# Kernel tuning notes

Measured on AMD Instinct MI355X. Metric: run time of the kernel, lower is better.

## Reference

```python
import jax, jax.numpy as jnp
import numpy as np

# Production-scale dims (see shape_source)
N = 100000      # nodes
E = 1600000     # shortest-path edges
I = 128         # in_channels
O = 128         # out_channels
K = 5           # max_distance
BN_EPS = 1e-5
GIN_EPS = 0.0   # eps=0.0, trainable_eps=False


def setup_inputs() -> dict:
    key = jax.random.key(0)
    ks = jax.random.split(key, 10)
    node_embeddings = jax.random.normal(ks[0], (N, I), dtype=jnp.float32)
    edge_index = jax.random.randint(ks[1], (2, E), 0, N)          # [2, E] row/col
    edge_weights = jax.random.randint(ks[2], (E,), 1, K + 1)      # SP distance in 1..K
    hop_coef = jax.random.normal(ks[3], (K,), dtype=jnp.float32)
    W1 = jax.random.normal(ks[4], (I, O), dtype=jnp.float32) / np.sqrt(I).astype(np.float32)
    b1 = jnp.zeros((O,), jnp.float32)
    gamma1 = jnp.ones((O,), jnp.float32)
    beta1 = jnp.zeros((O,), jnp.float32)
    W2 = jax.random.normal(ks[5], (O, O), dtype=jnp.float32) / np.sqrt(O).astype(np.float32)
    b2 = jnp.zeros((O,), jnp.float32)
    gamma2 = jnp.ones((O,), jnp.float32)
    beta2 = jnp.zeros((O,), jnp.float32)
    return {
        "node_embeddings": node_embeddings,
        "edge_index": edge_index,
        "edge_weights": edge_weights,
        "hop_coef": hop_coef,
        "W1": W1, "b1": b1, "gamma1": gamma1, "beta1": beta1,
        "W2": W2, "b2": b2, "gamma2": gamma2, "beta2": beta2,
    }


def _batch_norm(x, gamma, beta):
    # BatchNorm1d in training mode: batch mean, biased batch variance
    mean = x.mean(axis=0)
    var = x.var(axis=0)
    return gamma * (x - mean) * jax.lax.rsqrt(var + BN_EPS) + beta


def reference(node_embeddings, edge_index, edge_weights, hop_coef,
              W1, b1, gamma1, beta1, W2, b2, gamma2, beta2):
    # Fused form of the per-hop loop: each edge with SP distance d contributes
    # softmax(hop_coef)[d-1] * x[col] to out[row]. Identical math to K separate
    # sparse.mm's weighted by hop_weights and summed.
    hop_w = jax.nn.softmax(hop_coef)                               # [K]
    valid = (edge_weights >= 1) & (edge_weights <= K)
    w_e = jnp.where(valid, hop_w[jnp.clip(edge_weights - 1, 0, K - 1)], 0.0)  # [E]
    row, col = edge_index[0], edge_index[1]
    msgs = w_e[:, None] * node_embeddings[col]                     # [E, I] gather
    agg = jnp.zeros_like(node_embeddings).at[row].add(msgs)        # [N, I] scatter-add
    h = (1.0 + GIN_EPS) * node_embeddings + agg                    # GIN combine
    h = jax.nn.relu(_batch_norm(h @ W1 + b1, gamma1, beta1))
    h = jax.nn.relu(_batch_norm(h @ W2 + b2, gamma2, beta2))
    return h
```

## Files before the change

### kernel.cpp

```cpp
#include <hip/hip_runtime.h>
#include <hip/hip_bf16.h>


#define RCAP 64
#define P2B 256
#define BPB 4

typedef __attribute__((ext_vector_type(8))) short short8;
typedef __attribute__((ext_vector_type(4))) float f32x4;

__device__ inline unsigned short f2bf(float v) {
    unsigned int u = __float_as_uint(v);
    return (unsigned short)((u + 0x7fffu + ((u >> 16) & 1u)) >> 16);
}
__device__ inline float bf2f(unsigned int u) { return __uint_as_float(u << 16); }
__device__ inline float bflo(unsigned int u) { return __uint_as_float(u << 16); }
__device__ inline float bfhi(unsigned int u) { return __uint_as_float(u & 0xFFFF0000u); }

__global__ __launch_bounds__(256) void prep_k(
        const float* __restrict__ hc, float* __restrict__ hwp, float* __restrict__ sums,
        const float* __restrict__ W1, const float* __restrict__ W2,
        unsigned short* __restrict__ w1h, unsigned short* __restrict__ w1l,
        unsigned short* __restrict__ w2h, unsigned short* __restrict__ w2l,
        const float4* __restrict__ x4, uint4* __restrict__ xb, int K, long long n8) {
    int b = blockIdx.x, tid = threadIdx.x;
    if (b == 0) {
        sums[tid] = 0.f; sums[tid + 256] = 0.f;
        if (tid == 0) {
            float tmp[8];
            float m = -1e30f;
            for (int k = 0; k < K; ++k) m = fmaxf(m, hc[k]);
            float s = 0.f;
            for (int k = 0; k < K; ++k) { float e = __expf(hc[k] - m); tmp[k] = e; s += e; }
            float inv = 1.f / s;
            for (int k = 0; k < 8; ++k) hwp[k] = 0.f;
            for (int k = 0; k < K; ++k) hwp[k + 1] = tmp[k] * inv;
        }
        return;
    }
    if (b <= 2) {
        const float* W = (b == 2) ? W2 : W1;
        unsigned short* th = (b == 2) ? w2h : w1h;
        unsigned short* tl = (b == 2) ? w2l : w1l;
        for (int i = tid; i < 16384; i += 256) {
            int k = i >> 7, n = i & 127;
            float v = W[k * 128 + n];
            unsigned short hi = f2bf(v);
            th[n * 128 + k] = hi;
            tl[n * 128 + k] = f2bf(v - bf2f(hi));
        }
        return;
    }
    long long g = (long long)(b - 3) * 256 + tid;
    if (g >= n8) return;
    float4 a = x4[g * 2], c = x4[g * 2 + 1];
    union { unsigned short us[8]; uint4 v; } o;
    o.us[0] = f2bf(a.x); o.us[1] = f2bf(a.y); o.us[2] = f2bf(a.z); o.us[3] = f2bf(a.w);
    o.us[4] = f2bf(c.x); o.us[5] = f2bf(c.y); o.us[6] = f2bf(c.z); o.us[7] = f2bf(c.w);
    xb[g] = o.v;
}

__global__ __launch_bounds__(256) void count_k(const int* __restrict__ rows,
        int* __restrict__ C, int E, int per, int nbukp) {
    __shared__ int hist[128];
    int blk = blockIdx.x, tid = threadIdx.x;
    for (int i = tid; i < nbukp; i += 256) hist[i] = 0;
    __syncthreads();
    int e0 = blk * per, e1 = min(E, e0 + per);
    for (int e = e0 + tid; e < e1; e += 256)
        atomicAdd(&hist[rows[e] >> 10], 1);
    __syncthreads();
    for (int i = tid; i < nbukp; i += 256) C[blk * nbukp + i] = hist[i];
}

__global__ __launch_bounds__(256) void scan1_k(int* __restrict__ C,
        int* __restrict__ tot, int nbukp, int nblk) {
    __shared__ int buf[256];
    int b = blockIdx.x, tid = threadIdx.x;
    int v = (tid < nblk) ? C[tid * nbukp + b] : 0;
    buf[tid] = v;
    __syncthreads();
#pragma unroll
    for (int off = 1; off < 256; off <<= 1) {
        int t = (tid >= off) ? buf[tid - off] : 0;
        __syncthreads();
        buf[tid] += t;
        __syncthreads();
    }
    if (tid < nblk) C[tid * nbukp + b] = buf[tid] - v;
    if (tid == 255) tot[b] = buf[255];
}

__global__ __launch_bounds__(256) void scan2_k(const int* __restrict__ tot,
        int* __restrict__ bstart, int nbukp) {
    __shared__ int s[129];
    int tid = threadIdx.x;
    if (tid < nbukp) s[tid] = tot[tid];
    __syncthreads();
    if (tid == 0) {
        int run = 0;
        for (int b = 0; b < nbukp; b++) { int t = s[b]; bstart[b] = run; run += t; }
        bstart[nbukp] = run;
    }
}

__global__ __launch_bounds__(256) void scatter_k(const int* __restrict__ rows,
        const int* __restrict__ cols, const int* __restrict__ ew,
        const int* __restrict__ O, const int* __restrict__ bstart,
        unsigned* __restrict__ bucketed, int E, int per, int nbukp, int K) {
    __shared__ unsigned curs[128];
    int blk = blockIdx.x, tid = threadIdx.x;
    for (int i = tid; i < nbukp; i += 256)
        curs[i] = (unsigned)(O[blk * nbukp + i] + bstart[i]);
    __syncthreads();
    int e0 = blk * per, e1 = min(E, e0 + per);
    for (int e = e0 + tid; e < e1; e += 256) {
        int r = rows[e];
        int c = cols[e];
        int d = ew[e];
        if (d < 1 || d > K) d = 0;
        unsigned idx = atomicAdd(&curs[r >> 10], 1u);
        bucketed[idx] = (unsigned)d | ((unsigned)c << 3) | ((unsigned)(r & 1023) << 20);
    }
}

__global__ __launch_bounds__(256) void slot3_k(const unsigned* __restrict__ bucketed,
        const int* __restrict__ bstart, const float* __restrict__ hwp,
        int* __restrict__ cur, int2* __restrict__ staging, int nbukp) {
    int bucket = blockIdx.x % nbukp, sub = blockIdx.x / nbukp;
    int s0 = bstart[bucket], s1 = bstart[bucket + 1];
    int cnt = s1 - s0;
    int qlo = s0 + (int)((long long)cnt * sub / BPB);
    int qhi = s0 + (int)((long long)cnt * (sub + 1) / BPB);
    int rbase = bucket << 10;
    for (int e = qlo + threadIdx.x; e < qhi; e += 256) {
        unsigned u = bucketed[e];
        int d = u & 7;
        int col = (u >> 3) & 0x1FFFF;
        int row = rbase + (int)(u >> 20);
        float w = hwp[d];
        int s = atomicAdd(&cur[row], 1);
        if (s < RCAP)
            staging[((size_t)row << 6) + s] = make_int2(col, __float_as_int(w));
    }
}

__global__ __launch_bounds__(256) void slot_k(const int* __restrict__ rows,
        const int* __restrict__ cols, const int* __restrict__ ew,
        const float* __restrict__ hwp, int* __restrict__ cur,
        int2* __restrict__ staging, int E, int K) {
    int e = blockIdx.x * 256 + threadIdx.x;
    if (e >= E) return;
    int r = rows[e];
    int d = ew[e];
    if (d < 1 || d > K) d = 0;
    float w = hwp[d];
    int s = atomicAdd(&cur[r], 1);
    if (s < RCAP)
        staging[((size_t)r << 6) + s] = make_int2(cols[e], __float_as_int(w));
}

__global__ __launch_bounds__(256) void gather_k(
        const unsigned short* __restrict__ xb, const int2* __restrict__ staging,
        const int* __restrict__ cur, unsigned short* __restrict__ h, int N) {
    int wid = (blockIdx.x * 256 + threadIdx.x) >> 6;
    if (wid >= N) return;
    int lane = threadIdx.x & 63;
    int g4 = lane >> 4, li = lane & 15;
    int deg = __builtin_amdgcn_readfirstlane(cur[wid]);
    deg = min(deg, RCAP);
    const int2* ep = staging + ((size_t)wid << 6);
    const unsigned short* xrow = xb + li * 8;
    float a0 = 0.f, a1 = 0.f, a2 = 0.f, a3 = 0.f;
    float a4 = 0.f, a5 = 0.f, a6 = 0.f, a7 = 0.f;
    if (g4 == 0) {
        uint4 u = *(const uint4*)(xb + (size_t)wid * 128 + li * 8);
        a0 = bflo(u.x); a1 = bfhi(u.x); a2 = bflo(u.y); a3 = bfhi(u.y);
        a4 = bflo(u.z); a5 = bfhi(u.z); a6 = bflo(u.w); a7 = bfhi(u.w);
    }
    int j = 0;
    for (; j + 16 <= deg; j += 16) {
        int2 p0 = ep[j + g4];
        int2 p1 = ep[j + 4 + g4];
        int2 p2 = ep[j + 8 + g4];
        int2 p3 = ep[j + 12 + g4];
        uint4 u0 = *(const uint4*)(xrow + (size_t)p0.x * 128);
        uint4 u1 = *(const uint4*)(xrow + (size_t)p1.x * 128);
        uint4 u2 = *(const uint4*)(xrow + (size_t)p2.x * 128);
        uint4 u3 = *(const uint4*)(xrow + (size_t)p3.x * 128);
        float w0 = __int_as_float(p0.y), w1 = __int_as_float(p1.y);
        float w2 = __int_as_float(p2.y), w3 = __int_as_float(p3.y);
        a0 = fmaf(w0, bflo(u0.x), a0); a1 = fmaf(w0, bfhi(u0.x), a1);
        a2 = fmaf(w0, bflo(u0.y), a2); a3 = fmaf(w0, bfhi(u0.y), a3);
        a4 = fmaf(w0, bflo(u0.z), a4); a5 = fmaf(w0, bfhi(u0.z), a5);
        a6 = fmaf(w0, bflo(u0.w), a6); a7 = fmaf(w0, bfhi(u0.w), a7);
        a0 = fmaf(w1, bflo(u1.x), a0); a1 = fmaf(w1, bfhi(u1.x), a1);
        a2 = fmaf(w1, bflo(u1.y), a2); a3 = fmaf(w1, bfhi(u1.y), a3);
        a4 = fmaf(w1, bflo(u1.z), a4); a5 = fmaf(w1, bfhi(u1.z), a5);
        a6 = fmaf(w1, bflo(u1.w), a6); a7 = fmaf(w1, bfhi(u1.w), a7);
        a0 = fmaf(w2, bflo(u2.x), a0); a1 = fmaf(w2, bfhi(u2.x), a1);
        a2 = fmaf(w2, bflo(u2.y), a2); a3 = fmaf(w2, bfhi(u2.y), a3);
        a4 = fmaf(w2, bflo(u2.z), a4); a5 = fmaf(w2, bfhi(u2.z), a5);
        a6 = fmaf(w2, bflo(u2.w), a6); a7 = fmaf(w2, bfhi(u2.w), a7);
        a0 = fmaf(w3, bflo(u3.x), a0); a1 = fmaf(w3, bfhi(u3.x), a1);
        a2 = fmaf(w3, bflo(u3.y), a2); a3 = fmaf(w3, bfhi(u3.y), a3);
        a4 = fmaf(w3, bflo(u3.z), a4); a5 = fmaf(w3, bfhi(u3.z), a5);
        a6 = fmaf(w3, bflo(u3.w), a6); a7 = fmaf(w3, bfhi(u3.w), a7);
    }
    for (; j + 4 <= deg; j += 4) {
        int2 p = ep[j + g4];
        uint4 u = *(const uint4*)(xrow + (size_t)p.x * 128);
        float w = __int_as_float(p.y);
        a0 = fmaf(w, bflo(u.x), a0); a1 = fmaf(w, bfhi(u.x), a1);
        a2 = fmaf(w, bflo(u.y), a2); a3 = fmaf(w, bfhi(u.y), a3);
        a4 = fmaf(w, bflo(u.z), a4); a5 = fmaf(w, bfhi(u.z), a5);
        a6 = fmaf(w, bflo(u.w), a6); a7 = fmaf(w, bfhi(u.w), a7);
    }
    if (j < deg) {
        int jj = min(j + g4, deg - 1);
        int2 p = ep[jj];
        float w = (j + g4 < deg) ? __int_as_float(p.y) : 0.f;
        uint4 u = *(const uint4*)(xrow + (size_t)p.x * 128);
        a0 = fmaf(w, bflo(u.x), a0); a1 = fmaf(w, bfhi(u.x), a1);
        a2 = fmaf(w, bflo(u.y), a2); a3 = fmaf(w, bfhi(u.y), a3);
        a4 = fmaf(w, bflo(u.z), a4); a5 = fmaf(w, bfhi(u.z), a5);
        a6 = fmaf(w, bflo(u.w), a6); a7 = fmaf(w, bfhi(u.w), a7);
    }
    a0 += __shfl_xor(a0, 16); a1 += __shfl_xor(a1, 16);
    a2 += __shfl_xor(a2, 16); a3 += __shfl_xor(a3, 16);
    a4 += __shfl_xor(a4, 16); a5 += __shfl_xor(a5, 16);
    a6 += __shfl_xor(a6, 16); a7 += __shfl_xor(a7, 16);
    a0 += __shfl_xor(a0, 32); a1 += __shfl_xor(a1, 32);
    a2 += __shfl_xor(a2, 32); a3 += __shfl_xor(a3, 32);
    a4 += __shfl_xor(a4, 32); a5 += __shfl_xor(a5, 32);
    a6 += __shfl_xor(a6, 32); a7 += __shfl_xor(a7, 32);
    if (g4 == 0) {
        uint4 o;
        o.x = (unsigned int)f2bf(a0) | ((unsigned int)f2bf(a1) << 16);
        o.y = (unsigned int)f2bf(a2) | ((unsigned int)f2bf(a3) << 16);
        o.z = (unsigned int)f2bf(a4) | ((unsigned int)f2bf(a5) << 16);
        o.w = (unsigned int)f2bf(a6) | ((unsigned int)f2bf(a7) << 16);
        *(uint4*)(h + (size_t)wid * 128 + li * 8) = o;
    }
}

__global__ __launch_bounds__(256, 4) void gemm_mfma_k(
        const unsigned short* __restrict__ Ain,
        const unsigned short* __restrict__ Bhg, const unsigned short* __restrict__ Blg,
        const float* __restrict__ bias, unsigned short* __restrict__ zout,
        float* __restrict__ sum_out, float* __restrict__ sq_out, int N) {
    __shared__ unsigned short Bs[128 * 136];
    int tid = threadIdx.x;
    int wave = tid >> 6, lane = tid & 63;
    int n16 = lane & 15, q = lane >> 4;
    int rowbase = blockIdx.x * 128 + wave * 32;

    for (int i = tid; i < 2048; i += 256) {
        int n = i >> 4, c = i & 15;
        *(uint4*)&Bs[n * 136 + c * 8] = *(const uint4*)(Bhg + n * 128 + c * 8);
    }

    short8 afr[4][2];
#pragma unroll
    for (int kk = 0; kk < 4; kk++)
#pragma unroll
        for (int mt = 0; mt < 2; mt++) {
            int ar = rowbase + mt * 16 + n16;
            ar = min(ar, N - 1);
            afr[kk][mt] = *(const short8*)(Ain + (size_t)ar * 128 + kk * 32 + q * 8);
        }

    f32x4 acc[2][8];
#pragma unroll
    for (int mt = 0; mt < 2; mt++)
#pragma unroll
        for (int t = 0; t < 8; t++) acc[mt][t] = (f32x4){0.f, 0.f, 0.f, 0.f};

    __syncthreads();
    int ldsb = n16 * 136 + q * 8;
#pragma unroll
    for (int kk = 0; kk < 4; kk++)
#pragma unroll
        for (int t = 0; t < 8; t++) {
            short8 b = *(const short8*)&Bs[t * 16 * 136 + ldsb + kk * 32];
            acc[0][t] = __builtin_amdgcn_mfma_f32_16x16x32_bf16(afr[kk][0], b, acc[0][t], 0, 0, 0);
            acc[1][t] = __builtin_amdgcn_mfma_f32_16x16x32_bf16(afr[kk][1], b, acc[1][t], 0, 0, 0);
        }
    __syncthreads();
    for (int i = tid; i < 2048; i += 256) {
        int n = i >> 4, c = i & 15;
        *(uint4*)&Bs[n * 136 + c * 8] = *(const uint4*)(Blg + n * 128 + c * 8);
    }
    __syncthreads();
#pragma unroll
    for (int kk = 0; kk < 4; kk++)
#pragma unroll
        for (int t = 0; t < 8; t++) {
            short8 b = *(const short8*)&Bs[t * 16 * 136 + ldsb + kk * 32];
            acc[0][t] = __builtin_amdgcn_mfma_f32_16x16x32_bf16(afr[kk][0], b, acc[0][t], 0, 0, 0);
            acc[1][t] = __builtin_amdgcn_mfma_f32_16x16x32_bf16(afr[kk][1], b, acc[1][t], 0, 0, 0);
        }

    float csum[8], csq[8];
#pragma unroll
    for (int t = 0; t < 8; t++) { csum[t] = 0.f; csq[t] = 0.f; }
#pragma unroll
    for (int t = 0; t < 8; t++) {
        int col = n16 + 16 * t;
        float bv = bias[col];
#pragma unroll
        for (int mt = 0; mt < 2; mt++) {
#pragma unroll
            for (int r = 0; r < 4; r++) {
                int row = rowbase + mt * 16 + q * 4 + r;
                if (row < N) {
                    float v = acc[mt][t][r] + bv;
                    zout[(size_t)row * 128 + col] = f2bf(v);
                    csum[t] += v;
                    csq[t] += v * v;
                }
            }
        }
    }
#pragma unroll
    for (int t = 0; t < 8; t++) {
        csum[t] += __shfl_xor(csum[t], 16);
        csum[t] += __shfl_xor(csum[t], 32);
        csq[t] += __shfl_xor(csq[t], 16);
        csq[t] += __shfl_xor(csq[t], 32);
    }
    __syncthreads();
    float* red = (float*)Bs;
    if (q == 0) {
#pragma unroll
        for (int t = 0; t < 8; t++) {
            int col = n16 + 16 * t;
            red[wave * 128 + col] = csum[t];
            red[512 + wave * 128 + col] = csq[t];
        }
    }
    __syncthreads();
    if (tid < 128) {
        float s = 0.f, qq = 0.f;
#pragma unroll
        for (int w = 0; w < 4; w++) {
            s += red[w * 128 + tid];
            qq += red[512 + w * 128 + tid];
        }
        unsafeAtomicAdd(&sum_out[tid], s);
        unsafeAtomicAdd(&sq_out[tid], qq);
    }
}

__global__ __launch_bounds__(256) void bn1_k(const uint4* __restrict__ z,
        const float* __restrict__ sum, const float* __restrict__ sq,
        const float* __restrict__ gamma, const float* __restrict__ beta,
        uint4* __restrict__ out, long long n8, float invN) {
    __shared__ float sc[128], sh[128];
    int tid = threadIdx.x;
    if (tid < 128) {
        float mean = sum[tid] * invN;
        float var = fmaxf(sq[tid] * invN - mean * mean, 0.f);
        float s = gamma[tid] * rsqrtf(var + 1e-5f);
        sc[tid] = s;
        sh[tid] = beta[tid] - mean * s;
    }
    __syncthreads();
    long long g = (long long)blockIdx.x * 256 + tid;
    if (g >= n8) return;
    uint4 u = z[g];
    int cb = (int)((g * 8) & 127);
    float4 s0 = *(const float4*)&sc[cb], s1 = *(const float4*)&sc[cb + 4];
    float4 t0 = *(const float4*)&sh[cb], t1 = *(const float4*)&sh[cb + 4];
    float v0 = fmaxf(fmaf(bflo(u.x), s0.x, t0.x), 0.f);
    float v1 = fmaxf(fmaf(bfhi(u.x), s0.y, t0.y), 0.f);
    float v2 = fmaxf(fmaf(bflo(u.y), s0.z, t0.z), 0.f);
    float v3 = fmaxf(fmaf(bfhi(u.y), s0.w, t0.w), 0.f);
    float v4 = fmaxf(fmaf(bflo(u.z), s1.x, t1.x), 0.f);
    float v5 = fmaxf(fmaf(bfhi(u.z), s1.y, t1.y), 0.f);
    float v6 = fmaxf(fmaf(bflo(u.w), s1.z, t1.z), 0.f);
    float v7 = fmaxf(fmaf(bfhi(u.w), s1.w, t1.w), 0.f);
    uint4 o;
    o.x = (unsigned int)f2bf(v0) | ((unsigned int)f2bf(v1) << 16);
    o.y = (unsigned int)f2bf(v2) | ((unsigned int)f2bf(v3) << 16);
    o.z = (unsigned int)f2bf(v4) | ((unsigned int)f2bf(v5) << 16);
    o.w = (unsigned int)f2bf(v6) | ((unsigned int)f2bf(v7) << 16);
    out[g] = o;
}

__global__ __launch_bounds__(256) void bn2_k(const unsigned short* __restrict__ z2,
        const float* __restrict__ sum2, const float* __restrict__ sq2,
        const float* __restrict__ gamma, const float* __restrict__ beta,
        float* __restrict__ out, long long n8, float invN) {
    __shared__ float sc[128], sh[128];
    int tid = threadIdx.x;
    if (tid < 128) {
        float mean = sum2[tid] * invN;
        float var = fmaxf(sq2[tid] * invN - mean * mean, 0.f);
        float s = gamma[tid] * rsqrtf(var + 1e-5f);
        sc[tid] = s;
        sh[tid] = beta[tid] - mean * s;
    }
    __syncthreads();
    long long g = (long long)blockIdx.x * 256 + tid;
    if (g >= n8) return;
    uint4 u = ((const uint4*)z2)[g];
    int cb = (int)((g * 8) & 127);
    float4 s0 = *(const float4*)&sc[cb], s1 = *(const float4*)&sc[cb + 4];
    float4 t0 = *(const float4*)&sh[cb], t1 = *(const float4*)&sh[cb + 4];
    float4 o0, o1;
    o0.x = fmaxf(fmaf(bflo(u.x), s0.x, t0.x), 0.f);
    o0.y = fmaxf(fmaf(bfhi(u.x), s0.y, t0.y), 0.f);
    o0.z = fmaxf(fmaf(bflo(u.y), s0.z, t0.z), 0.f);
    o0.w = fmaxf(fmaf(bfhi(u.y), s0.w, t0.w), 0.f);
    o1.x = fmaxf(fmaf(bflo(u.z), s1.x, t1.x), 0.f);
    o1.y = fmaxf(fmaf(bfhi(u.z), s1.y, t1.y), 0.f);
    o1.z = fmaxf(fmaf(bflo(u.w), s1.z, t1.z), 0.f);
    o1.w = fmaxf(fmaf(bfhi(u.w), s1.w, t1.w), 0.f);
    ((float4*)out)[g * 2] = o0;
    ((float4*)out)[g * 2 + 1] = o1;
}

extern "C" void kernel_launch(void* const* d_in, const int* in_sizes, int n_in,
                              void* d_out, int out_size, void* d_ws, size_t ws_size,
                              hipStream_t stream) {
    const float* x   = (const float*)d_in[0];
    const int*   ei  = (const int*)d_in[1];
    const int*   ew  = (const int*)d_in[2];
    const float* hc  = (const float*)d_in[3];
    const float* W1  = (const float*)d_in[4];
    const float* b1  = (const float*)d_in[5];
    const float* g1  = (const float*)d_in[6];
    const float* be1 = (const float*)d_in[7];
    const float* W2  = (const float*)d_in[8];
    const float* b2  = (const float*)d_in[9];
    const float* g2  = (const float*)d_in[10];
    const float* be2 = (const float*)d_in[11];

    int N = in_sizes[0] / 128;
    int E = in_sizes[2];
    int K = in_sizes[3];
    size_t NF = (size_t)N * 128;
    long long n8 = (long long)(NF / 8);
    int NX = (int)((n8 + 255) / 256);

    unsigned short* h = (unsigned short*)d_ws;
    unsigned short* xb = h + NF;
    unsigned short* z1 = xb;
    unsigned short* a1 = h;
    unsigned short* z2 = xb;
    int2* staging = (int2*)(xb + NF);
    int* cur = (int*)(staging + (size_t)N * RCAP);
    unsigned short* w1h = (unsigned short*)(cur + N);
    unsigned short* w1l = w1h + 16384;
    unsigned short* w2h = w1l + 16384;
    unsigned short* w2l = w2h + 16384;
    float* hwp = (float*)(w2l + 16384);
    float* sums = hwp + 8;
    float* sum1 = sums, *sq1 = sums + 128, *sum2 = sums + 256, *sq2 = sums + 384;
    int nbuk  = (N + 1023) >> 10;
    int nbukp = (nbuk + 7) & ~7;
    int* C = (int*)(sums + 512);
    int* bstart = C + (size_t)P2B * nbukp;
    int* tot = bstart + nbukp + 1;
    unsigned* bucketed = (unsigned*)(tot + nbukp);
    size_t ws_need = (size_t)((char*)(bucketed + E) - (char*)d_ws);
    bool use_bucketed = (nbukp <= 128) && (N <= (1 << 17)) && (K <= 7)
                        && (ws_need <= ws_size);

    float invN = 1.0f / (float)N;

    hipMemsetAsync(cur, 0, (size_t)N * sizeof(int), stream);

    prep_k<<<3 + NX, 256, 0, stream>>>(hc, hwp, sums, W1, W2,
        w1h, w1l, w2h, w2l, (const float4*)x, (uint4*)xb, K, n8);
    if (use_bucketed) {
        int per = (E + P2B - 1) / P2B;
        count_k<<<P2B, 256, 0, stream>>>(ei, C, E, per, nbukp);
        scan1_k<<<nbukp, 256, 0, stream>>>(C, tot, nbukp, P2B);
        scan2_k<<<1, 256, 0, stream>>>(tot, bstart, nbukp);
        scatter_k<<<P2B, 256, 0, stream>>>(ei, ei + E, ew, C, bstart, bucketed,
                                           E, per, nbukp, K);
        slot3_k<<<nbukp * BPB, 256, 0, stream>>>(bucketed, bstart, hwp, cur, staging, nbukp);
    } else {
        slot_k<<<(E + 255) / 256, 256, 0, stream>>>(ei, ei + E, ew, hwp, cur, staging, E, K);
    }
    {
        long long tot_thr = (long long)N * 64;
        gather_k<<<(int)((tot_thr + 255) / 256), 256, 0, stream>>>(xb, staging, cur, h, N);
    }
    int gblocks = (N + 127) / 128;
    gemm_mfma_k<<<gblocks, 256, 0, stream>>>(h, w1h, w1l, b1, z1, sum1, sq1, N);
    bn1_k<<<NX, 256, 0, stream>>>((const uint4*)z1, sum1, sq1, g1, be1,
        (uint4*)a1, n8, invN);
    gemm_mfma_k<<<gblocks, 256, 0, stream>>>(a1, w2h, w2l, b2, z2, sum2, sq2, N);
    bn2_k<<<NX, 256, 0, stream>>>(z2, sum2, sq2, g2, be2, (float*)d_out, n8, invN);
}
```

Before: 444.1 us.

## Fuse BN1+ReLU into second GEMM, pack staging edges, parallelize scans

```diff
diff --git a/kernel.cpp b/kernel.cpp
--- a/kernel.cpp
+++ b/kernel.cpp
@@ -70,14 +70,14 @@
     for (int e = e0 + tid; e < e1; e += 256)
         atomicAdd(&hist[rows[e] >> 10], 1);
     __syncthreads();
-    for (int i = tid; i < nbukp; i += 256) C[blk * nbukp + i] = hist[i];
+    for (int i = tid; i < nbukp; i += 256) C[i * P2B + blk] = hist[i];
 }
 
 __global__ __launch_bounds__(256) void scan1_k(int* __restrict__ C,
         int* __restrict__ tot, int nbukp, int nblk) {
     __shared__ int buf[256];
     int b = blockIdx.x, tid = threadIdx.x;
-    int v = (tid < nblk) ? C[tid * nbukp + b] : 0;
+    int v = (tid < nblk) ? C[b * P2B + tid] : 0;
     buf[tid] = v;
     __syncthreads();
 #pragma unroll
@@ -87,21 +87,26 @@
         buf[tid] += t;
         __syncthreads();
     }
-    if (tid < nblk) C[tid * nbukp + b] = buf[tid] - v;
+    if (tid < nblk) C[b * P2B + tid] = buf[tid] - v;
     if (tid == 255) tot[b] = buf[255];
 }
 
 __global__ __launch_bounds__(256) void scan2_k(const int* __restrict__ tot,
         int* __restrict__ bstart, int nbukp) {
-    __shared__ int s[129];
+    __shared__ int buf[256];
     int tid = threadIdx.x;
-    if (tid < nbukp) s[tid] = tot[tid];
-    __syncthreads();
-    if (tid == 0) {
-        int run = 0;
-        for (int b = 0; b < nbukp; b++) { int t = s[b]; bstart[b] = run; run += t; }
-        bstart[nbukp] = run;
-    }
+    int v = (tid < nbukp) ? tot[tid] : 0;
+    buf[tid] = v;
+    __syncthreads();
+#pragma unroll
+    for (int off = 1; off < 256; off <<= 1) {
+        int t = (tid >= off) ? buf[tid - off] : 0;
+        __syncthreads();
+        buf[tid] += t;
+        __syncthreads();
+    }
+    if (tid < nbukp) bstart[tid] = buf[tid] - v;
+    if (tid == 0) bstart[nbukp] = buf[nbukp - 1];
 }
 
 __global__ __launch_bounds__(256) void scatter_k(const int* __restrict__ rows,
@@ -111,7 +116,7 @@
     __shared__ unsigned curs[128];
     int blk = blockIdx.x, tid = threadIdx.x;
     for (int i = tid; i < nbukp; i += 256)
-        curs[i] = (unsigned)(O[blk * nbukp + i] + bstart[i]);
+        curs[i] = (unsigned)(O[i * P2B + blk] + bstart[i]);
     __syncthreads();
     int e0 = blk * per, e1 = min(E, e0 + per);
     for (int e = e0 + tid; e < e1; e += 256) {
@@ -125,8 +130,8 @@
 }
 
 __global__ __launch_bounds__(256) void slot3_k(const unsigned* __restrict__ bucketed,
-        const int* __restrict__ bstart, const float* __restrict__ hwp,
-        int* __restrict__ cur, int2* __restrict__ staging, int nbukp) {
+        const int* __restrict__ bstart, int* __restrict__ cur,
+        unsigned* __restrict__ staging, int nbukp) {
     int bucket = blockIdx.x % nbukp, sub = blockIdx.x / nbukp;
     int s0 = bstart[bucket], s1 = bstart[bucket + 1];
     int cnt = s1 - s0;
@@ -135,41 +140,41 @@
     int rbase = bucket << 10;
     for (int e = qlo + threadIdx.x; e < qhi; e += 256) {
         unsigned u = bucketed[e];
-        int d = u & 7;
-        int col = (u >> 3) & 0x1FFFF;
         int row = rbase + (int)(u >> 20);
-        float w = hwp[d];
         int s = atomicAdd(&cur[row], 1);
         if (s < RCAP)
-            staging[((size_t)row << 6) + s] = make_int2(col, __float_as_int(w));
+            staging[((size_t)row << 6) + s] = u & 0xFFFFFu;
     }
 }
 
 __global__ __launch_bounds__(256) void slot_k(const int* __restrict__ rows,
         const int* __restrict__ cols, const int* __restrict__ ew,
-        const float* __restrict__ hwp, int* __restrict__ cur,
-        int2* __restrict__ staging, int E, int K) {
+        int* __restrict__ cur, unsigned* __restrict__ staging, int E, int K) {
     int e = blockIdx.x * 256 + threadIdx.x;
     if (e >= E) return;
     int r = rows[e];
     int d = ew[e];
     if (d < 1 || d > K) d = 0;
-    float w = hwp[d];
     int s = atomicAdd(&cur[r], 1);
     if (s < RCAP)
-        staging[((size_t)r << 6) + s] = make_int2(cols[e], __float_as_int(w));
+        staging[((size_t)r << 6) + s] = (unsigned)d | ((unsigned)cols[e] << 3);
 }
 
 __global__ __launch_bounds__(256) void gather_k(
-        const unsigned short* __restrict__ xb, const int2* __restrict__ staging,
-        const int* __restrict__ cur, unsigned short* __restrict__ h, int N) {
-    int wid = (blockIdx.x * 256 + threadIdx.x) >> 6;
+        const unsigned short* __restrict__ xb, const unsigned* __restrict__ staging,
+        const int* __restrict__ cur, const float* __restrict__ hwp,
+        unsigned short* __restrict__ h, int N) {
+    __shared__ float hwl[8];
+    int tid = threadIdx.x;
+    if (tid < 8) hwl[tid] = hwp[tid];
+    __syncthreads();
+    int wid = (blockIdx.x * 256 + tid) >> 6;
     if (wid >= N) return;
-    int lane = threadIdx.x & 63;
+    int lane = tid & 63;
     int g4 = lane >> 4, li = lane & 15;
     int deg = __builtin_amdgcn_readfirstlane(cur[wid]);
     deg = min(deg, RCAP);
-    const int2* ep = staging + ((size_t)wid << 6);
+    const unsigned* ep = staging + ((size_t)wid << 6);
     const unsigned short* xrow = xb + li * 8;
     float a0 = 0.f, a1 = 0.f, a2 = 0.f, a3 = 0.f;
     float a4 = 0.f, a5 = 0.f, a6 = 0.f, a7 = 0.f;
@@ -180,16 +185,16 @@
     }
     int j = 0;
     for (; j + 16 <= deg; j += 16) {
-        int2 p0 = ep[j + g4];
-        int2 p1 = ep[j + 4 + g4];
-        int2 p2 = ep[j + 8 + g4];
-        int2 p3 = ep[j + 12 + g4];
-        uint4 u0 = *(const uint4*)(xrow + (size_t)p0.x * 128);
-        uint4 u1 = *(const uint4*)(xrow + (size_t)p1.x * 128);
-        uint4 u2 = *(const uint4*)(xrow + (size_t)p2.x * 128);
-        uint4 u3 = *(const uint4*)(xrow + (size_t)p3.x * 128);
-        float w0 = __int_as_float(p0.y), w1 = __int_as_float(p1.y);
-        float w2 = __int_as_float(p2.y), w3 = __int_as_float(p3.y);
+        unsigned p0 = ep[j + g4];
+        unsigned p1 = ep[j + 4 + g4];
+        unsigned p2 = ep[j + 8 + g4];
+        unsigned p3 = ep[j + 12 + g4];
+        uint4 u0 = *(const uint4*)(xrow + (size_t)(p0 >> 3) * 128);
+        uint4 u1 = *(const uint4*)(xrow + (size_t)(p1 >> 3) * 128);
+        uint4 u2 = *(const uint4*)(xrow + (size_t)(p2 >> 3) * 128);
+        uint4 u3 = *(const uint4*)(xrow + (size_t)(p3 >> 3) * 128);
+        float w0 = hwl[p0 & 7], w1 = hwl[p1 & 7];
+        float w2 = hwl[p2 & 7], w3 = hwl[p3 & 7];
         a0 = fmaf(w0, bflo(u0.x), a0); a1 = fmaf(w0, bfhi(u0.x), a1);
         a2 = fmaf(w0, bflo(u0.y), a2); a3 = fmaf(w0, bfhi(u0.y), a3);
         a4 = fmaf(w0, bflo(u0.z), a4); a5 = fmaf(w0, bfhi(u0.z), a5);
@@ -208,9 +213,9 @@
         a6 = fmaf(w3, bflo(u3.w), a6); a7 = fmaf(w3, bfhi(u3.w), a7);
     }
     for (; j + 4 <= deg; j += 4) {
-        int2 p = ep[j + g4];
-        uint4 u = *(const uint4*)(xrow + (size_t)p.x * 128);
-        float w = __int_as_float(p.y);
+        unsigned p = ep[j + g4];
+        uint4 u = *(const uint4*)(xrow + (size_t)(p >> 3) * 128);
+        float w = hwl[p & 7];
         a0 = fmaf(w, bflo(u.x), a0); a1 = fmaf(w, bfhi(u.x), a1);
         a2 = fmaf(w, bflo(u.y), a2); a3 = fmaf(w, bfhi(u.y), a3);
         a4 = fmaf(w, bflo(u.z), a4); a5 = fmaf(w, bfhi(u.z), a5);
@@ -218,9 +223,9 @@
     }
     if (j < deg) {
         int jj = min(j + g4, deg - 1);
-        int2 p = ep[jj];
-        float w = (j + g4 < deg) ? __int_as_float(p.y) : 0.f;
-        uint4 u = *(const uint4*)(xrow + (size_t)p.x * 128);
+        unsigned p = ep[jj];
+        float w = (j + g4 < deg) ? hwl[p & 7] : 0.f;
+        uint4 u = *(const uint4*)(xrow + (size_t)(p >> 3) * 128);
         a0 = fmaf(w, bflo(u.x), a0); a1 = fmaf(w, bfhi(u.x), a1);
         a2 = fmaf(w, bflo(u.y), a2); a3 = fmaf(w, bfhi(u.y), a3);
         a4 = fmaf(w, bflo(u.z), a4); a5 = fmaf(w, bfhi(u.z), a5);
@@ -352,40 +357,132 @@
     }
 }
 
-__global__ __launch_bounds__(256) void bn1_k(const uint4* __restrict__ z,
-        const float* __restrict__ sum, const float* __restrict__ sq,
+__global__ __launch_bounds__(256, 4) void gemm_mfma_bn_k(
+        const unsigned short* __restrict__ Zin,
+        const float* __restrict__ sum_in, const float* __restrict__ sq_in,
         const float* __restrict__ gamma, const float* __restrict__ beta,
-        uint4* __restrict__ out, long long n8, float invN) {
+        float invN,
+        const unsigned short* __restrict__ Bhg, const unsigned short* __restrict__ Blg,
+        const float* __restrict__ bias, unsigned short* __restrict__ zout,
+        float* __restrict__ sum_out, float* __restrict__ sq_out, int N) {
+    __shared__ unsigned short Bs[128 * 136];
     __shared__ float sc[128], sh[128];
     int tid = threadIdx.x;
+    int wave = tid >> 6, lane = tid & 63;
+    int n16 = lane & 15, q = lane >> 4;
+    int rowbase = blockIdx.x * 128 + wave * 32;
+
+    for (int i = tid; i < 2048; i += 256) {
+        int n = i >> 4, c = i & 15;
+        *(uint4*)&Bs[n * 136 + c * 8] = *(const uint4*)(Bhg + n * 128 + c * 8);
+    }
     if (tid < 128) {
-        float mean = sum[tid] * invN;
-        float var = fmaxf(sq[tid] * invN - mean * mean, 0.f);
+        float mean = sum_in[tid] * invN;
+        float var = fmaxf(sq_in[tid] * invN - mean * mean, 0.f);
         float s = gamma[tid] * rsqrtf(var + 1e-5f);
         sc[tid] = s;
         sh[tid] = beta[tid] - mean * s;
     }
     __syncthreads();
-    long long g = (long long)blockIdx.x * 256 + tid;
-    if (g >= n8) return;
-    uint4 u = z[g];
-    int cb = (int)((g * 8) & 127);
-    float4 s0 = *(const float4*)&sc[cb], s1 = *(const float4*)&sc[cb + 4];
-    float4 t0 = *(const float4*)&sh[cb], t1 = *(const float4*)&sh[cb + 4];
-    float v0 = fmaxf(fmaf(bflo(u.x), s0.x, t0.x), 0.f);
-    float v1 = fmaxf(fmaf(bfhi(u.x), s0.y, t0.y), 0.f);
-    float v2 = fmaxf(fmaf(bflo(u.y), s0.z, t0.z), 0.f);
-    float v3 = fmaxf(fmaf(bfhi(u.y), s0.w, t0.w), 0.f);
-    float v4 = fmaxf(fmaf(bflo(u.z), s1.x, t1.x), 0.f);
-    float v5 = fmaxf(fmaf(bfhi(u.z), s1.y, t1.y), 0.f);
-    float v6 = fmaxf(fmaf(bflo(u.w), s1.z, t1.z), 0.f);
-    float v7 = fmaxf(fmaf(bfhi(u.w), s1.w, t1.w), 0.f);
-    uint4 o;
-    o.x = (unsigned int)f2bf(v0) | ((unsigned int)f2bf(v1) << 16);
-    o.y = (unsigned int)f2bf(v2) | ((unsigned int)f2bf(v3) << 16);
-    o.z = (unsigned int)f2bf(v4) | ((unsigned int)f2bf(v5) << 16);
-    o.w = (unsigned int)f2bf(v6) | ((unsigned int)f2bf(v7) << 16);
-    out[g] = o;
+
+    short8 afr[4][2];
+#pragma unroll
+    for (int kk = 0; kk < 4; kk++)
+#pragma unroll
+        for (int mt = 0; mt < 2; mt++) {
+            int ar = rowbase + mt * 16 + n16;
+            ar = min(ar, N - 1);
+            short8 raw = *(const short8*)(Zin + (size_t)ar * 128 + kk * 32 + q * 8);
+            short8 outv;
+#pragma unroll
+            for (int i = 0; i < 8; i++) {
+                int col = kk * 32 + q * 8 + i;
+                float f = bf2f((unsigned short)raw[i]);
+                float v = fmaxf(fmaf(f, sc[col], sh[col]), 0.f);
+                outv[i] = (short)f2bf(v);
+            }
+            afr[kk][mt] = outv;
+        }
+
+    f32x4 acc[2][8];
+#pragma unroll
+    for (int mt = 0; mt < 2; mt++)
+#pragma unroll
+        for (int t = 0; t < 8; t++) acc[mt][t] = (f32x4){0.f, 0.f, 0.f, 0.f};
+
+    int ldsb = n16 * 136 + q * 8;
+#pragma unroll
+    for (int kk = 0; kk < 4; kk++)
+#pragma unroll
+        for (int t = 0; t < 8; t++) {
+            short8 b = *(const short8*)&Bs[t * 16 * 136 + ldsb + kk * 32];
+            acc[0][t] = __builtin_amdgcn_mfma_f32_16x16x32_bf16(afr[kk][0], b, acc[0][t], 0, 0, 0);
+            acc[1][t] = __builtin_amdgcn_mfma_f32_16x16x32_bf16(afr[kk][1], b, acc[1][t], 0, 0, 0);
+        }
+    __syncthreads();
+    for (int i = tid; i < 2048; i += 256) {
+        int n = i >> 4, c = i & 15;
+        *(uint4*)&Bs[n * 136 + c * 8] = *(const uint4*)(Blg + n * 128 + c * 8);
+    }
+    __syncthreads();
+#pragma unroll
+    for (int kk = 0; kk < 4; kk++)
+#pragma unroll
+        for (int t = 0; t < 8; t++) {
+            short8 b = *(const short8*)&Bs[t * 16 * 136 + ldsb + kk * 32];
+            acc[0][t] = __builtin_amdgcn_mfma_f32_16x16x32_bf16(afr[kk][0], b, acc[0][t], 0, 0, 0);
+            acc[1][t] = __builtin_amdgcn_mfma_f32_16x16x32_bf16(afr[kk][1], b, acc[1][t], 0, 0, 0);
+        }
+
+    float csum[8], csq[8];
+#pragma unroll
+    for (int t = 0; t < 8; t++) { csum[t] = 0.f; csq[t] = 0.f; }
+#pragma unroll
+    for (int t = 0; t < 8; t++) {
+        int col = n16 + 16 * t;
+        float bv = bias[col];
+#pragma unroll
+        for (int mt = 0; mt < 2; mt++) {
+#pragma unroll
+            for (int r = 0; r < 4; r++) {
+                int row = rowbase + mt * 16 + q * 4 + r;
+                if (row < N) {
+                    float v = acc[mt][t][r] + bv;
+                    zout[(size_t)row * 128 + col] = f2bf(v);
+                    csum[t] += v;
+                    csq[t] += v * v;
+                }
+            }
+        }
+    }
+#pragma unroll
+    for (int t = 0; t < 8; t++) {
+        csum[t] += __shfl_xor(csum[t], 16);
+        csum[t] += __shfl_xor(csum[t], 32);
+        csq[t] += __shfl_xor(csq[t], 16);
+        csq[t] += __shfl_xor(csq[t], 32);
+    }
+    __syncthreads();
+    float* red = (float*)Bs;
+    if (q == 0) {
+#pragma unroll
+        for (int t = 0; t < 8; t++) {
+            int col = n16 + 16 * t;
+            red[wave * 128 + col] = csum[t];
+            red[512 + wave * 128 + col] = csq[t];
+        }
+    }
+    __syncthreads();
+    if (tid < 128) {
+        float s = 0.f, qq = 0.f;
+#pragma unroll
+        for (int w = 0; w < 4; w++) {
+            s += red[w * 128 + tid];
+            qq += red[512 + w * 128 + tid];
+        }
+        unsafeAtomicAdd(&sum_out[tid], s);
+        unsafeAtomicAdd(&sq_out[tid], qq);
+    }
 }
 
 __global__ __launch_bounds__(256) void bn2_k(const unsigned short* __restrict__ z2,
@@ -447,9 +544,8 @@
     unsigned short* h = (unsigned short*)d_ws;
     unsigned short* xb = h + NF;
     unsigned short* z1 = xb;
-    unsigned short* a1 = h;
-    unsigned short* z2 = xb;
-    int2* staging = (int2*)(xb + NF);
+    unsigned short* z2 = h;
+    unsigned* staging = (unsigned*)(xb + NF);
     int* cur = (int*)(staging + (size_t)N * RCAP);
     unsigned short* w1h = (unsigned short*)(cur + N);
     unsigned short* w1l = w1h + 16384;
@@ -461,7 +557,7 @@
     int nbuk  = (N + 1023) >> 10;
     int nbukp = (nbuk + 7) & ~7;
     int* C = (int*)(sums + 512);
-    int* bstart = C + (size_t)P2B * nbukp;
+    int* bstart = C + (size_t)nbukp * P2B;
     int* tot = bstart + nbukp + 1;
     unsigned* bucketed = (unsigned*)(tot + nbukp);
     size_t ws_need = (size_t)((char*)(bucketed + E) - (char*)d_ws);
@@ -481,18 +577,18 @@
         scan2_k<<<1, 256, 0, stream>>>(tot, bstart, nbukp);
         scatter_k<<<P2B, 256, 0, stream>>>(ei, ei + E, ew, C, bstart, bucketed,
                                            E, per, nbukp, K);
-        slot3_k<<<nbukp * BPB, 256, 0, stream>>>(bucketed, bstart, hwp, cur, staging, nbukp);
+        slot3_k<<<nbukp * BPB, 256, 0, stream>>>(bucketed, bstart, cur, staging, nbukp);
     } else {
-        slot_k<<<(E + 255) / 256, 256, 0, stream>>>(ei, ei + E, ew, hwp, cur, staging, E, K);
+        slot_k<<<(E + 255) / 256, 256, 0, stream>>>(ei, ei + E, ew, cur, staging, E, K);
     }
     {
         long long tot_thr = (long long)N * 64;
-        gather_k<<<(int)((tot_thr + 255) / 256), 256, 0, stream>>>(xb, staging, cur, h, N);
+        gather_k<<<(int)((tot_thr + 255) / 256), 256, 0, stream>>>(
+            xb, staging, cur, hwp, h, N);
     }
     int gblocks = (N + 127) / 128;
     gemm_mfma_k<<<gblocks, 256, 0, stream>>>(h, w1h, w1l, b1, z1, sum1, sq1, N);
-    bn1_k<<<NX, 256, 0, stream>>>((const uint4*)z1, sum1, sq1, g1, be1,
-        (uint4*)a1, n8, invN);
-    gemm_mfma_k<<<gblocks, 256, 0, stream>>>(a1, w2h, w2l, b2, z2, sum2, sq2, N);
+    gemm_mfma_bn_k<<<gblocks, 256, 0, stream>>>(z1, sum1, sq1, g1, be1, invN,
+        w2h, w2l, b2, z2, sum2, sq2, N);
     bn2_k<<<NX, 256, 0, stream>>>(z2, sum2, sq2, g2, be2, (float*)d_out, n8, invN);
 }
```

Result: faster. 434.3 us (-2.2%).
